# Optimization experiments

Hardware: AMD Instinct MI355X
Metric: run time of the kernel (lower is better)

Reference implementation:

```python
import jax, jax.numpy as jnp
import numpy as np

TEMP = 0.5
EPS = 1e-12  # torch F.normalize eps


def setup_inputs() -> dict:
    key = jax.random.key(0)
    k1, k2, k3 = jax.random.split(key, 3)
    B, D = 2048, 128
    z = jax.random.normal(k1, (B, D), dtype=jnp.float32)
    z_aug = jax.random.normal(k2, (B, D), dtype=jnp.float32)
    labels = jax.random.randint(k3, (B,), 0, 2, dtype=jnp.int64)
    return {"z": z, "z_aug": z_aug, "labels": labels}


def _l2_normalize(x):
    n = jnp.linalg.norm(x, axis=1, keepdims=True)
    return x / jnp.maximum(n, EPS)


def _pucon_loss(z, z_aug, labels):
    B = z.shape[0]
    z = _l2_normalize(z)
    z_aug = _l2_normalize(z_aug)

    s00 = (z @ z.T) / TEMP          # [B, B]
    s01 = (z @ z_aug.T) / TEMP
    s10 = (z_aug @ z.T) / TEMP
    s11 = (z_aug @ z_aug.T) / TEMP

    eye = jnp.eye(B, dtype=bool)

    # ---- SelfSupConLoss (reduction='none'): CE over rows with own-diagonal
    # removed from the 00/11 blocks; removal == masking with -inf for CE.
    neg_inf = jnp.array(-jnp.inf, dtype=s00.dtype)
    logits = jnp.concatenate([
        jnp.concatenate([s01, jnp.where(eye, neg_inf, s00)], axis=1),
        jnp.concatenate([s10, jnp.where(eye, neg_inf, s11)], axis=1),
    ], axis=0)                       # [2B, 2B]
    pos = jnp.concatenate([jnp.diagonal(s01), jnp.diagonal(s10)])  # [2B]
    lse = jax.scipy.special.logsumexp(logits, axis=1)
    unsup = lse - pos                # [2B] per-sample NT-Xent loss

    # ---- SupConLoss (reduction='none')
    M = jnp.concatenate([
        jnp.concatenate([s00, s01], axis=1),
        jnp.concatenate([s10, s11], axis=1),
    ], axis=0)                       # [2B, 2B]
    mx = jax.lax.stop_gradient(jnp.max(M, axis=1, keepdims=True))
    Ms = M - mx
    mask = ~jnp.eye(2 * B, dtype=bool)
    e = jnp.where(mask, jnp.exp(Ms), 0.0)
    denom = jnp.sum(e, axis=1, keepdims=True)
    # -log(exp(Ms)/denom) on off-diagonal entries, 0 on diagonal
    nll = jnp.where(mask, jnp.log(denom) - Ms, 0.0)
    eq = labels[:, None] == labels[None, :]
    eq2 = jnp.tile(eq, (2, 2))       # [2B, 2B] bool
    sup = jnp.sum(nll * eq2, axis=1) / (jnp.sum(eq2, axis=1) - 1)  # [2B]

    # ---- PU combination: positives use sup loss, unlabeled use unsup loss
    lab2 = jnp.tile(labels, 2)       # [2B]
    pos_m = (lab2 == 1)
    neg_m = (lab2 == 0)
    n_p = jnp.sum(pos_m)
    n_u = jnp.sum(neg_m)
    total = jnp.maximum(n_p + n_u, 1)
    loss = (jnp.sum(jnp.where(pos_m, sup, 0.0)) +
            jnp.sum(jnp.where(neg_m, unsup, 0.0))) / total
    return jnp.where(n_p == 0, jnp.mean(unsup), loss)


def reference(z, z_aug, labels):
    return _pucon_loss(z, z_aug, labels)
```

## Files before the change

kernel.cpp:

```cpp
#include <hip/hip_runtime.h>
#include <hip/hip_bf16.h>

#define Bsz 2048
#define Dim 128
#define Nrows 4096

typedef float f32x4 __attribute__((ext_vector_type(4)));
typedef __bf16 bf16x8 __attribute__((ext_vector_type(8)));

#define GLD_LDS16(gp, lp)                                                        \
    __builtin_amdgcn_global_load_lds(                                            \
        (const __attribute__((address_space(1))) void*)(gp),                     \
        (__attribute__((address_space(3))) void*)(lp), 16, 0, 0)


__global__ __launch_bounds__(256) void k_norm(const float* __restrict__ z,
                                              const float* __restrict__ za,
                                              const long long* __restrict__ labels,
                                              __bf16* __restrict__ U,
                                              float* __restrict__ w1p,
                                              float* __restrict__ wallp,
                                              int* __restrict__ c1out) {
    const int wid = threadIdx.x >> 6, lane = threadIdx.x & 63;
    __shared__ float s1[4][128];
    __shared__ float s0[4][128];
    float a1x = 0.f, a1y = 0.f, a0x = 0.f, a0y = 0.f;
    #pragma unroll
    for (int pass = 0; pass < 4; pass++) {
        const int r = blockIdx.x * 16 + pass * 4 + wid;
        const float* src = (r < Bsz) ? (z + (size_t)r * Dim) : (za + (size_t)(r - Bsz) * Dim);
        float2 x = reinterpret_cast<const float2*>(src)[lane];
        float ss = x.x * x.x + x.y * x.y;
        #pragma unroll
        for (int m = 1; m < 64; m <<= 1) ss += __shfl_xor(ss, m);
        const float sc = 1.0f / fmaxf(sqrtf(ss), 1e-12f);
        const float u0 = x.x * sc, u1 = x.y * sc;
        __bf16* dst = U + (size_t)r * Dim + 2 * lane;
        dst[0] = (__bf16)u0;
        dst[1] = (__bf16)u1;
        const float lf = (labels[r & (Bsz - 1)] == 1) ? 1.f : 0.f;
        a0x += u0; a0y += u1;
        a1x = fmaf(lf, u0, a1x); a1y = fmaf(lf, u1, a1y);
    }
    s1[wid][2 * lane] = a1x; s1[wid][2 * lane + 1] = a1y;
    s0[wid][2 * lane] = a0x; s0[wid][2 * lane + 1] = a0y;
    __syncthreads();
    const int t = threadIdx.x;
    if (t < 128) {
        w1p[blockIdx.x * 128 + t]   = s1[0][t] + s1[1][t] + s1[2][t] + s1[3][t];
        wallp[blockIdx.x * 128 + t] = s0[0][t] + s0[1][t] + s0[2][t] + s0[3][t];
    }
    if (blockIdx.x == 0) {
        __shared__ int ci[256];
        int c = 0;
        #pragma unroll
        for (int k = 0; k < 8; k++) c += (int)labels[t * 8 + k];
        ci[t] = c;
        __syncthreads();
        for (int s = 128; s > 0; s >>= 1) {
            if (t < s) ci[t] += ci[t + s];
            __syncthreads();
        }
        if (t == 0) c1out[0] = ci[0];
    }
}

__global__ __launch_bounds__(256, 2) void k_gram(const __bf16* __restrict__ U,
                                                 const float* __restrict__ w1p,
                                                 const float* __restrict__ wallp,
                                                 float* __restrict__ part,
                                                 float* __restrict__ w1,
                                                 float* __restrict__ wall) {
    if (blockIdx.x == 1024) {
        const int t = threadIdx.x;
        const int d = t & 127;
        const float* src = (t < 128) ? w1p : wallp;
        float acc = 0.f;
        #pragma unroll 8
        for (int k = 0; k < 256; k++) acc += src[k * 128 + d];
        if (t < 128) w1[d] = acc; else wall[d] = acc;
        return;
    }

    __shared__ __bf16 Ai[128 * 128];
    __shared__ __bf16 Aj[128 * 128];

    const int iblk = blockIdx.x >> 5, jblk = blockIdx.x & 31;
    const int ibase = iblk * 128, jbase = jblk * 128;
    const int w = threadIdx.x >> 6, lane = threadIdx.x & 63;
    const int wi = w & 1, wj = w >> 1;
    const int l15 = lane & 15, l4 = lane >> 4;

    {
        const int c = lane & 15, rsub = lane >> 4;
        #pragma unroll
        for (int it = 0; it < 8; it++) {
            const int rl = w * 32 + it * 4 + rsub;
            const int soff = (c ^ (rl & 7)) * 8;
            GLD_LDS16(U + (size_t)(ibase + rl) * Dim + soff, Ai + (size_t)(w * 32 + it * 4) * 128);
            GLD_LDS16(U + (size_t)(jbase + rl) * Dim + soff, Aj + (size_t)(w * 32 + it * 4) * 128);
        }
    }
    __syncthreads();

    bf16x8 b[4][4];
    #pragma unroll
    for (int bt = 0; bt < 4; bt++)
        #pragma unroll
        for (int ks = 0; ks < 4; ks++)
            b[bt][ks] = *reinterpret_cast<const bf16x8*>(
                Ai + ((wi * 64 + bt * 16 + l15) * 16 + ((ks * 4 + l4) ^ (l15 & 7))) * 8);

    float dsum[4] = {0.f, 0.f, 0.f, 0.f};
    const float KE1 = 2.8853900817779268f;
    const float KE0 = -2.8853900817779268f;

    #pragma unroll
    for (int at = 0; at < 4; at++) {
        bf16x8 a[4];
        #pragma unroll
        for (int ks = 0; ks < 4; ks++)
            a[ks] = *reinterpret_cast<const bf16x8*>(
                Aj + ((wj * 64 + at * 16 + l15) * 16 + ((ks * 4 + l4) ^ (l15 & 7))) * 8);
        const int jt = jbase + wj * 64 + at * 16;

        #pragma unroll
        for (int bt = 0; bt < 4; bt++) {
            f32x4 acc = {0.f, 0.f, 0.f, 0.f};
            #pragma unroll
            for (int ks = 0; ks < 4; ks++)
                acc = __builtin_amdgcn_mfma_f32_16x16x32_bf16(a[ks], b[bt][ks], acc, 0, 0, 0);
            const bool dg = (jt == ibase + wi * 64 + bt * 16);
            #pragma unroll
            for (int q = 0; q < 4; q++) {
                float e = exp2f(fmaf(acc[q], KE1, KE0));
                if (dg && (l15 == l4 * 4 + q)) e = 0.f;
                dsum[bt] += e;
            }
        }
    }

    const int strip = jblk * 2 + wj;
    #pragma unroll
    for (int bt = 0; bt < 4; bt++) {
        float v0 = dsum[bt];
        v0 += __shfl_xor(v0, 16);
        v0 += __shfl_xor(v0, 32);
        if (l4 == 0)
            part[(ibase + wi * 64 + bt * 16 + l15) * 64 + strip] = v0;
    }
}

__global__ __launch_bounds__(256) void k_row(const __bf16* __restrict__ U,
                                             const long long* __restrict__ labels,
                                             const int* __restrict__ c1p,
                                             const float* __restrict__ part,
                                             const float* __restrict__ w1,
                                             const float* __restrict__ wall,
                                             float* __restrict__ rowC,
                                             float* __restrict__ rowU) {
    const int wid = threadIdx.x >> 6, lane = threadIdx.x & 63;
    const int c1 = *c1p;
    const float w1a = w1[2 * lane], w1b = w1[2 * lane + 1];
    const float wa  = wall[2 * lane], wb = wall[2 * lane + 1];
    float cs = 0.f, us = 0.f;
    #pragma unroll
    for (int rr = 0; rr < 4; rr++) {
        const int i = blockIdx.x * 16 + wid * 4 + rr;
        const int partner = (i < Bsz) ? i + Bsz : i - Bsz;
        float dn = part[i * 64 + lane];
        const float u0 = (float)U[(size_t)i * Dim + 2 * lane];
        const float u1 = (float)U[(size_t)i * Dim + 2 * lane + 1];
        const float p0 = (float)U[(size_t)partner * Dim + 2 * lane];
        const float p1 = (float)U[(size_t)partner * Dim + 2 * lane + 1];
        float d1 = u0 * w1a + u1 * w1b;
        float da = u0 * wa + u1 * wb;
        float ds = u0 * u0 + u1 * u1;
        float dp = u0 * p0 + u1 * p1;
        #pragma unroll
        for (int m = 1; m < 64; m <<= 1) {
            dn += __shfl_xor(dn, m);
            d1 += __shfl_xor(d1, m);
            da += __shfl_xor(da, m);
            ds += __shfl_xor(ds, m);
            dp += __shfl_xor(dp, m);
        }
        if (lane == 0) {
            const long long lb = labels[i & (Bsz - 1)];
            const float lnD = logf(dn) + 2.0f;
            const float uns = lnD - 2.0f * dp;
            const float cnt = 2.f * (float)((lb == 1) ? c1 : (Bsz - c1));
            const float sii = 2.f * ds;
            const float sumeq = ((lb == 1) ? 2.f * d1 : 2.f * (da - d1)) - sii;
            const float sup = lnD - sumeq / (cnt - 1.f);
            cs += (lb == 1) ? sup : uns;
            us += uns;
        }
    }
    __shared__ float wcs[4], wus[4];
    if (lane == 0) { wcs[wid] = cs; wus[wid] = us; }
    __syncthreads();
    if (threadIdx.x == 0) {
        rowC[blockIdx.x] = wcs[0] + wcs[1] + wcs[2] + wcs[3];
        rowU[blockIdx.x] = wus[0] + wus[1] + wus[2] + wus[3];
    }
}

__global__ __launch_bounds__(256) void k_comb(const float* __restrict__ rowC,
                                              const float* __restrict__ rowU,
                                              const int* __restrict__ c1p,
                                              float* __restrict__ out) {
    __shared__ float sc[256], su[256];
    const int t = threadIdx.x;
    sc[t] = rowC[t];
    su[t] = rowU[t];
    __syncthreads();
    for (int s = 128; s > 0; s >>= 1) {
        if (t < s) { sc[t] += sc[t + s]; su[t] += su[t + s]; }
        __syncthreads();
    }
    if (t == 0) out[0] = ((*c1p > 0) ? sc[0] : su[0]) / (float)Nrows;
}

extern "C" void kernel_launch(void* const* d_in, const int* in_sizes, int n_in,
                              void* d_out, int out_size, void* d_ws, size_t ws_size,
                              hipStream_t stream) {
    const float* z  = (const float*)d_in[0];
    const float* za = (const float*)d_in[1];
    const long long* labels = (const long long*)d_in[2];

    char* ws = (char*)d_ws;
    __bf16* U     = (__bf16*)(ws);
    float*  part  = (float*)(ws + (1u << 20));
    float*  w1p   = (float*)(ws + (2u << 20));
    float*  wallp = (float*)(ws + (2u << 20) + (128u << 10));
    float*  w1    = (float*)(ws + (2u << 20) + (256u << 10));
    float*  wall  = (float*)(ws + (2u << 20) + (256u << 10) + 512);
    int*    c1    = (int*)  (ws + (2u << 20) + (256u << 10) + 1024);
    float*  rowC  = (float*)(ws + (2u << 20) + (257u << 10));
    float*  rowU  = (float*)(ws + (2u << 20) + (258u << 10));
    float*  out   = (float*)d_out;

    hipLaunchKernelGGL(k_norm, dim3(256),  dim3(256), 0, stream, z, za, labels, U, w1p, wallp, c1);
    hipLaunchKernelGGL(k_gram, dim3(1025), dim3(256), 0, stream, U, w1p, wallp, part, w1, wall);
    hipLaunchKernelGGL(k_row,  dim3(256),  dim3(256), 0, stream, U, labels, c1, part, w1, wall, rowC, rowU);
    hipLaunchKernelGGL(k_comb, dim3(1),    dim3(256), 0, stream, rowC, rowU, c1, out);
}
```

Before: 34.23 us.

## Exploit Gram matrix symmetry to compute only upper-triangular tiles

The 4096x4096 Gram exp-sum kernel now launches only the 528 upper-triangular 128x128 tiles plus the reduction block. Each off-diagonal tile writes both its row partial sums and its column partial sums, the column sums coming from shuffle reductions, so the mirrored tile is never computed. The direct global-to-LDS loads are replaced with ordinary vector loads and swizzled LDS stores, and diagonal tiles load only one operand. This roughly halves the MFMA and exp work, at the cost of extra shuffles, extra partial-sum stores and a serial loop that maps block index to tile.

```diff
diff --git a/kernel.cpp b/kernel.cpp
--- a/kernel.cpp
+++ b/kernel.cpp
@@ -7,11 +7,6 @@
 
 typedef float f32x4 __attribute__((ext_vector_type(4)));
 typedef __bf16 bf16x8 __attribute__((ext_vector_type(8)));
-
-#define GLD_LDS16(gp, lp)                                                        \
-    __builtin_amdgcn_global_load_lds(                                            \
-        (const __attribute__((address_space(1))) void*)(gp),                     \
-        (__attribute__((address_space(3))) void*)(lp), 16, 0, 0)
 
 
 __global__ __launch_bounds__(256) void k_norm(const float* __restrict__ z,
@@ -71,7 +66,7 @@
                                                  float* __restrict__ part,
                                                  float* __restrict__ w1,
                                                  float* __restrict__ wall) {
-    if (blockIdx.x == 1024) {
+    if (blockIdx.x == 0) {
         const int t = threadIdx.x;
         const int d = t & 127;
         const float* src = (t < 128) ? w1p : wallp;
@@ -82,23 +77,32 @@
         return;
     }
 
+    int bidx = blockIdx.x - 1, ib = 0;
+    while (bidx >= 32 - ib) { bidx -= 32 - ib; ib++; }
+    const int jb = ib + bidx;
+    const bool diag = (ib == jb);
+
     __shared__ __bf16 Ai[128 * 128];
     __shared__ __bf16 Aj[128 * 128];
-
-    const int iblk = blockIdx.x >> 5, jblk = blockIdx.x & 31;
-    const int ibase = iblk * 128, jbase = jblk * 128;
+    const __bf16* AjP = diag ? Ai : Aj;
+
+    const int ibase = ib * 128, jbase = jb * 128;
     const int w = threadIdx.x >> 6, lane = threadIdx.x & 63;
     const int wi = w & 1, wj = w >> 1;
     const int l15 = lane & 15, l4 = lane >> 4;
 
     {
-        const int c = lane & 15, rsub = lane >> 4;
+        const int p = lane & 15, rsub = lane >> 4;
         #pragma unroll
         for (int it = 0; it < 8; it++) {
             const int rl = w * 32 + it * 4 + rsub;
-            const int soff = (c ^ (rl & 7)) * 8;
-            GLD_LDS16(U + (size_t)(ibase + rl) * Dim + soff, Ai + (size_t)(w * 32 + it * 4) * 128);
-            GLD_LDS16(U + (size_t)(jbase + rl) * Dim + soff, Aj + (size_t)(w * 32 + it * 4) * 128);
+            const int dst = (rl * 16 + (p ^ (rl & 7))) * 8;
+            bf16x8 vi = *reinterpret_cast<const bf16x8*>(U + (size_t)(ibase + rl) * Dim + p * 8);
+            *reinterpret_cast<bf16x8*>(Ai + dst) = vi;
+            if (!diag) {
+                bf16x8 vj = *reinterpret_cast<const bf16x8*>(U + (size_t)(jbase + rl) * Dim + p * 8);
+                *reinterpret_cast<bf16x8*>(Aj + dst) = vj;
+            }
         }
     }
     __syncthreads();
@@ -114,6 +118,7 @@
     float dsum[4] = {0.f, 0.f, 0.f, 0.f};
     const float KE1 = 2.8853900817779268f;
     const float KE0 = -2.8853900817779268f;
+    const int stripI = ib * 2 + wi;
 
     #pragma unroll
     for (int at = 0; at < 4; at++) {
@@ -121,8 +126,9 @@
         #pragma unroll
         for (int ks = 0; ks < 4; ks++)
             a[ks] = *reinterpret_cast<const bf16x8*>(
-                Aj + ((wj * 64 + at * 16 + l15) * 16 + ((ks * 4 + l4) ^ (l15 & 7))) * 8);
+                AjP + ((wj * 64 + at * 16 + l15) * 16 + ((ks * 4 + l4) ^ (l15 & 7))) * 8);
         const int jt = jbase + wj * 64 + at * 16;
+        float jq[4] = {0.f, 0.f, 0.f, 0.f};
 
         #pragma unroll
         for (int bt = 0; bt < 4; bt++) {
@@ -136,18 +142,37 @@
                 float e = exp2f(fmaf(acc[q], KE1, KE0));
                 if (dg && (l15 == l4 * 4 + q)) e = 0.f;
                 dsum[bt] += e;
-            }
-        }
-    }
-
-    const int strip = jblk * 2 + wj;
+                jq[q] += e;
+            }
+        }
+
+        if (!diag) {
+            #pragma unroll
+            for (int q = 0; q < 4; q++) {
+                float v = jq[q];
+                v += __shfl_xor(v, 1);
+                v += __shfl_xor(v, 2);
+                v += __shfl_xor(v, 4);
+                v += __shfl_xor(v, 8);
+                jq[q] = v;
+            }
+            if (l15 == 0) {
+                const int jgl = jbase + wj * 64 + at * 16 + l4 * 4;
+                #pragma unroll
+                for (int q = 0; q < 4; q++)
+                    part[(jgl + q) * 64 + stripI] = jq[q];
+            }
+        }
+    }
+
+    const int stripJ = jb * 2 + wj;
     #pragma unroll
     for (int bt = 0; bt < 4; bt++) {
         float v0 = dsum[bt];
         v0 += __shfl_xor(v0, 16);
         v0 += __shfl_xor(v0, 32);
         if (l4 == 0)
-            part[(ibase + wi * 64 + bt * 16 + l15) * 64 + strip] = v0;
+            part[(ibase + wi * 64 + bt * 16 + l15) * 64 + stripJ] = v0;
     }
 }
 
@@ -241,8 +266,8 @@
     float*  rowU  = (float*)(ws + (2u << 20) + (258u << 10));
     float*  out   = (float*)d_out;
 
-    hipLaunchKernelGGL(k_norm, dim3(256),  dim3(256), 0, stream, z, za, labels, U, w1p, wallp, c1);
-    hipLaunchKernelGGL(k_gram, dim3(1025), dim3(256), 0, stream, U, w1p, wallp, part, w1, wall);
-    hipLaunchKernelGGL(k_row,  dim3(256),  dim3(256), 0, stream, U, labels, c1, part, w1, wall, rowC, rowU);
-    hipLaunchKernelGGL(k_comb, dim3(1),    dim3(256), 0, stream, rowC, rowU, c1, out);
-}
+    hipLaunchKernelGGL(k_norm, dim3(256), dim3(256), 0, stream, z, za, labels, U, w1p, wallp, c1);
+    hipLaunchKernelGGL(k_gram, dim3(529), dim3(256), 0, stream, U, w1p, wallp, part, w1, wall);
+    hipLaunchKernelGGL(k_row,  dim3(256), dim3(256), 0, stream, U, labels, c1, part, w1, wall, rowC, rowU);
+    hipLaunchKernelGGL(k_comb, dim3(1),   dim3(256), 0, stream, rowC, rowU, c1, out);
+}
```

After: 32.05 us. 1.07x faster.

## Process two j-tiles per gram block with register-staged prefetch of second tile

Applied to the files above, without the earlier changes.

Each gram block now handles one 128-row i-tile against two 128-row j-tiles, halving the grid. The i-tile operands are loaded straight from global memory into registers instead of through LDS. The j-tiles are staged through registers into swizzled LDS, with the second tile's global loads issued before computing the first, so the load latency can overlap MFMA work. This reuses the i-tile operands across twice as much work. In exchange it raises register pressure, runs fewer blocks, and gives up the direct global-to-LDS load path.

```diff
diff --git a/kernel.cpp b/kernel.cpp
--- a/kernel.cpp
+++ b/kernel.cpp
@@ -7,11 +7,6 @@
 
 typedef float f32x4 __attribute__((ext_vector_type(4)));
 typedef __bf16 bf16x8 __attribute__((ext_vector_type(8)));
-
-#define GLD_LDS16(gp, lp)                                                        \
-    __builtin_amdgcn_global_load_lds(                                            \
-        (const __attribute__((address_space(1))) void*)(gp),                     \
-        (__attribute__((address_space(3))) void*)(lp), 16, 0, 0)
 
 
 __global__ __launch_bounds__(256) void k_norm(const float* __restrict__ z,
@@ -71,7 +66,7 @@
                                                  float* __restrict__ part,
                                                  float* __restrict__ w1,
                                                  float* __restrict__ wall) {
-    if (blockIdx.x == 1024) {
+    if (blockIdx.x == 0) {
         const int t = threadIdx.x;
         const int d = t & 127;
         const float* src = (t < 128) ? w1p : wallp;
@@ -82,73 +77,96 @@
         return;
     }
 
-    __shared__ __bf16 Ai[128 * 128];
-    __shared__ __bf16 Aj[128 * 128];
-
-    const int iblk = blockIdx.x >> 5, jblk = blockIdx.x & 31;
-    const int ibase = iblk * 128, jbase = jblk * 128;
+    __shared__ __bf16 Aj0[128 * 128];
+    __shared__ __bf16 Aj1[128 * 128];
+
+    const int ib = (blockIdx.x - 1) >> 4;
+    const int jc = (blockIdx.x - 1) & 15;
+    const int ibase = ib * 128;
+    const int jbase0 = jc * 256, jbase1 = jc * 256 + 128;
     const int w = threadIdx.x >> 6, lane = threadIdx.x & 63;
     const int wi = w & 1, wj = w >> 1;
     const int l15 = lane & 15, l4 = lane >> 4;
+    const int p = lane & 15, rsub = lane >> 4;
+
+    bf16x8 b[4][4];
+    #pragma unroll
+    for (int bt = 0; bt < 4; bt++)
+        #pragma unroll
+        for (int ks = 0; ks < 4; ks++)
+            b[bt][ks] = *reinterpret_cast<const bf16x8*>(
+                U + (size_t)(ibase + wi * 64 + bt * 16 + l15) * Dim + (ks * 4 + l4) * 8);
 
     {
-        const int c = lane & 15, rsub = lane >> 4;
+        bf16x8 st[8];
         #pragma unroll
         for (int it = 0; it < 8; it++) {
             const int rl = w * 32 + it * 4 + rsub;
-            const int soff = (c ^ (rl & 7)) * 8;
-            GLD_LDS16(U + (size_t)(ibase + rl) * Dim + soff, Ai + (size_t)(w * 32 + it * 4) * 128);
-            GLD_LDS16(U + (size_t)(jbase + rl) * Dim + soff, Aj + (size_t)(w * 32 + it * 4) * 128);
-        }
-    }
-    __syncthreads();
-
-    bf16x8 b[4][4];
-    #pragma unroll
-    for (int bt = 0; bt < 4; bt++)
-        #pragma unroll
-        for (int ks = 0; ks < 4; ks++)
-            b[bt][ks] = *reinterpret_cast<const bf16x8*>(
-                Ai + ((wi * 64 + bt * 16 + l15) * 16 + ((ks * 4 + l4) ^ (l15 & 7))) * 8);
-
-    float dsum[4] = {0.f, 0.f, 0.f, 0.f};
+            st[it] = *reinterpret_cast<const bf16x8*>(U + (size_t)(jbase0 + rl) * Dim + p * 8);
+        }
+        #pragma unroll
+        for (int it = 0; it < 8; it++) {
+            const int rl = w * 32 + it * 4 + rsub;
+            *reinterpret_cast<bf16x8*>(Aj0 + (rl * 16 + (p ^ (rl & 7))) * 8) = st[it];
+        }
+    }
+    __syncthreads();
+
+    bf16x8 st1[8];
+    #pragma unroll
+    for (int it = 0; it < 8; it++) {
+        const int rl = w * 32 + it * 4 + rsub;
+        st1[it] = *reinterpret_cast<const bf16x8*>(U + (size_t)(jbase1 + rl) * Dim + p * 8);
+    }
+
     const float KE1 = 2.8853900817779268f;
     const float KE0 = -2.8853900817779268f;
 
-    #pragma unroll
-    for (int at = 0; at < 4; at++) {
-        bf16x8 a[4];
-        #pragma unroll
-        for (int ks = 0; ks < 4; ks++)
-            a[ks] = *reinterpret_cast<const bf16x8*>(
-                Aj + ((wj * 64 + at * 16 + l15) * 16 + ((ks * 4 + l4) ^ (l15 & 7))) * 8);
-        const int jt = jbase + wj * 64 + at * 16;
-
-        #pragma unroll
-        for (int bt = 0; bt < 4; bt++) {
-            f32x4 acc = {0.f, 0.f, 0.f, 0.f};
+    auto compute = [&](const __bf16* Aj, int jbase, int strip) {
+        float dsum[4] = {0.f, 0.f, 0.f, 0.f};
+        #pragma unroll
+        for (int at = 0; at < 4; at++) {
+            bf16x8 a[4];
             #pragma unroll
             for (int ks = 0; ks < 4; ks++)
-                acc = __builtin_amdgcn_mfma_f32_16x16x32_bf16(a[ks], b[bt][ks], acc, 0, 0, 0);
-            const bool dg = (jt == ibase + wi * 64 + bt * 16);
+                a[ks] = *reinterpret_cast<const bf16x8*>(
+                    Aj + ((wj * 64 + at * 16 + l15) * 16 + ((ks * 4 + l4) ^ (l15 & 7))) * 8);
+            const int jt = jbase + wj * 64 + at * 16;
             #pragma unroll
-            for (int q = 0; q < 4; q++) {
-                float e = exp2f(fmaf(acc[q], KE1, KE0));
-                if (dg && (l15 == l4 * 4 + q)) e = 0.f;
-                dsum[bt] += e;
+            for (int bt = 0; bt < 4; bt++) {
+                f32x4 acc = {0.f, 0.f, 0.f, 0.f};
+                #pragma unroll
+                for (int ks = 0; ks < 4; ks++)
+                    acc = __builtin_amdgcn_mfma_f32_16x16x32_bf16(a[ks], b[bt][ks], acc, 0, 0, 0);
+                const bool dg = (jt == ibase + wi * 64 + bt * 16);
+                #pragma unroll
+                for (int q = 0; q < 4; q++) {
+                    float e = exp2f(fmaf(acc[q], KE1, KE0));
+                    if (dg && (l15 == l4 * 4 + q)) e = 0.f;
+                    dsum[bt] += e;
+                }
             }
         }
-    }
-
-    const int strip = jblk * 2 + wj;
-    #pragma unroll
-    for (int bt = 0; bt < 4; bt++) {
-        float v0 = dsum[bt];
-        v0 += __shfl_xor(v0, 16);
-        v0 += __shfl_xor(v0, 32);
-        if (l4 == 0)
-            part[(ibase + wi * 64 + bt * 16 + l15) * 64 + strip] = v0;
-    }
+        #pragma unroll
+        for (int bt = 0; bt < 4; bt++) {
+            float v0 = dsum[bt];
+            v0 += __shfl_xor(v0, 16);
+            v0 += __shfl_xor(v0, 32);
+            if (l4 == 0)
+                part[(ibase + wi * 64 + bt * 16 + l15) * 64 + strip] = v0;
+        }
+    };
+
+    compute(Aj0, jbase0, jc * 4 + wj);
+
+    #pragma unroll
+    for (int it = 0; it < 8; it++) {
+        const int rl = w * 32 + it * 4 + rsub;
+        *reinterpret_cast<bf16x8*>(Aj1 + (rl * 16 + (p ^ (rl & 7))) * 8) = st1[it];
+    }
+    __syncthreads();
+
+    compute(Aj1, jbase1, jc * 4 + 2 + wj);
 }
 
 __global__ __launch_bounds__(256) void k_row(const __bf16* __restrict__ U,
@@ -241,8 +259,8 @@
     float*  rowU  = (float*)(ws + (2u << 20) + (258u << 10));
     float*  out   = (float*)d_out;
 
-    hipLaunchKernelGGL(k_norm, dim3(256),  dim3(256), 0, stream, z, za, labels, U, w1p, wallp, c1);
-    hipLaunchKernelGGL(k_gram, dim3(1025), dim3(256), 0, stream, U, w1p, wallp, part, w1, wall);
-    hipLaunchKernelGGL(k_row,  dim3(256),  dim3(256), 0, stream, U, labels, c1, part, w1, wall, rowC, rowU);
-    hipLaunchKernelGGL(k_comb, dim3(1),    dim3(256), 0, stream, rowC, rowU, c1, out);
-}
+    hipLaunchKernelGGL(k_norm, dim3(256), dim3(256), 0, stream, z, za, labels, U, w1p, wallp, c1);
+    hipLaunchKernelGGL(k_gram, dim3(513), dim3(256), 0, stream, U, w1p, wallp, part, w1, wall);
+    hipLaunchKernelGGL(k_row,  dim3(256), dim3(256), 0, stream, U, labels, c1, part, w1, wall, rowC, rowU);
+    hipLaunchKernelGGL(k_comb, dim3(1),   dim3(256), 0, stream, rowC, rowU, c1, out);
+}
```

Result: faster. 31.49 us (-8.0%).
